# Performance work log

Hardware: AMD Instinct MI355X
Metric: run time of the kernel (lower is better)

The kernel has to match this reference:

```python
import jax, jax.numpy as jnp
import numpy as np

N = 1024          # num_rois == nongt_dim
FEAT = 1024       # feat_dim
EMB = 64          # emb_dim
G = 16            # group == fc_dim
DG = FEAT // G    # dim_group = 64
CLS = 80          # coco classes
EPS_POS = 1e-3
EPS_AFF = 1e-6


def setup_inputs() -> dict:
    key = jax.random.key(0)
    ks = jax.random.split(key, 12)
    # valid boxes: xmin,ymin in [0,500), width/height in [1,101)
    xymin = jax.random.uniform(ks[0], (N, 2), dtype=jnp.float32) * 500.0
    wh = 1.0 + jax.random.uniform(ks[1], (N, 2), dtype=jnp.float32) * 100.0
    bbox = jnp.concatenate([xymin[:, :1], xymin[:, 1:], xymin[:, :1] + wh[:, :1], xymin[:, 1:] + wh[:, 1:]], axis=1)
    roi_feat = jax.random.normal(ks[2], (N, FEAT), dtype=jnp.float32)
    s = lambda d: 1.0 / np.sqrt(d)
    return {
        "bbox": bbox,
        "roi_feat": roi_feat,
        "W_pos": jax.random.normal(ks[3], (EMB, G), dtype=jnp.float32) * s(EMB),
        "b_pos": jnp.zeros((G,), jnp.float32),
        "Wq": jax.random.normal(ks[4], (FEAT, FEAT), dtype=jnp.float32) * s(FEAT),
        "bq": jnp.zeros((FEAT,), jnp.float32),
        "Wk": jax.random.normal(ks[5], (FEAT, FEAT), dtype=jnp.float32) * s(FEAT),
        "bk": jnp.zeros((FEAT,), jnp.float32),
        # grouped 1x1 conv: groups=16, in/group=FEAT=1024, out/group=DG=64 -> [G, DG, FEAT]
        "W_conv": jax.random.normal(ks[6], (G, DG, FEAT), dtype=jnp.float32) * s(FEAT),
        "b_conv": jnp.zeros((FEAT,), jnp.float32),
        "W_ro": jax.random.normal(ks[7], (FEAT, CLS), dtype=jnp.float32) * s(FEAT),
        "b_ro": jnp.zeros((CLS,), jnp.float32),
    }


def _position_matrix(bbox):
    xmin, ymin, xmax, ymax = bbox[:, 0], bbox[:, 1], bbox[:, 2], bbox[:, 3]
    w = xmax - xmin + 1.0
    h = ymax - ymin + 1.0
    cx = 0.5 * (xmin + xmax)
    cy = 0.5 * (ymin + ymax)

    def log_clamped(d):
        d = jnp.where(jnp.abs(d) < EPS_POS, EPS_POS, d)
        return jnp.log(jnp.abs(d))

    dx = log_clamped((cx[:, None] - cx[None, :]) / w[:, None])
    dy = log_clamped((cy[:, None] - cy[None, :]) / h[:, None])
    dw = log_clamped(w[:, None] / w[None, :])
    dh = log_clamped(h[:, None] / h[None, :])
    return jnp.stack([dx, dy, dw, dh], axis=2)  # [N, N, 4]


def _position_embedding(pos_mat, feat_dim=EMB, wave_length=1000.0):
    feat_range = jnp.arange(feat_dim // 8, dtype=jnp.float32)          # 8 freqs
    dim_mat = jnp.power(jnp.float32(wave_length), (8.0 / feat_dim) * feat_range)
    div = pos_mat[..., None] / dim_mat                                  # [N, N, 4, 8]
    emb = jnp.concatenate([jnp.sin(div), jnp.cos(div)], axis=-1)        # [N, N, 4, 16]
    return emb.reshape(pos_mat.shape[0], pos_mat.shape[1], feat_dim)    # [N, N, 64]


def reference(bbox, roi_feat, W_pos, b_pos, Wq, bq, Wk, bk, W_conv, b_conv, W_ro, b_ro):
    n = roi_feat.shape[0]
    pos_emb = _position_embedding(_position_matrix(bbox))               # [N, N, 64]
    aff_w = jax.nn.relu(pos_emb @ W_pos + b_pos)                        # [N, N, G]
    aff_w = jnp.transpose(aff_w, (0, 2, 1))                             # [N, G, N]

    q = (roi_feat @ Wq + bq).reshape(n, G, DG)                          # [N, G, DG]
    k = (roi_feat @ Wk + bk).reshape(n, G, DG)
    aff = jnp.einsum('igd,jgd->igj', q, k) * (1.0 / np.sqrt(DG))        # [N, G, N]

    aff_w = jnp.where(aff_w < EPS_AFF, EPS_AFF, aff_w)
    sm = jax.nn.softmax(jnp.log(aff_w) + aff, axis=2)                   # [N, G, N]

    out_t = jnp.einsum('igj,jd->igd', sm, roi_feat)                     # [N, G, FEAT]
    lin = jnp.einsum('igd,gkd->igk', out_t, W_conv).reshape(n, FEAT) + b_conv
    res = roi_feat + lin                                                # [N, FEAT]
    logits = res.sum(axis=0, keepdims=True) @ W_ro + b_ro               # [1, CLS]
    return jax.nn.sigmoid(logits)
```

## Files before the change

kernel.cpp:

```cpp
#include <hip/hip_runtime.h>
#include <hip/hip_bf16.h>
#include <math.h>

#define NN   1024
#define GG   16
#define DGD  64
#define CLS  80
#define SPLIT 4
#define JT_PER 4

typedef __attribute__((ext_vector_type(8))) short short8;
typedef __attribute__((ext_vector_type(4))) float f32x4;
typedef _Float16 half8 __attribute__((ext_vector_type(8)));

__device__ inline void split2t(float x, ushort& h, ushort& l) {
  uint u = __float_as_uint(x);
  h = (ushort)(u >> 16);
  float r = x - __uint_as_float(u & 0xFFFF0000u);
  l = (ushort)(__float_as_uint(r) >> 16);
}

__device__ inline ushort f32tof16(float x) {
  _Float16 h = (_Float16)x;
  return *(ushort*)&h;
}
__device__ inline float f16tof32(ushort u) {
  _Float16 h; *(ushort*)&h = u;
  return (float)h;
}

__device__ inline int wslot(int r, int kc) {
  return ((r >> 4) << 6) + ((kc & 3) << 4) + ((r & 15) ^ ((kc & 3) << 2));
}
__device__ inline int rslot(int f, int lane) {
  return (f << 6) + ((lane >> 4) << 4) + ((lane & 15) ^ ((lane >> 4) << 2));
}

__global__ __launch_bounds__(256) void prep_k(
    const float* __restrict__ roi, ushort* __restrict__ roiH, ushort* __restrict__ roiL,
    const float* __restrict__ Wc,  ushort* __restrict__ WcH,  ushort* __restrict__ WcL,
    const float* __restrict__ Wq,  const float* __restrict__ Wk,
    ushort* __restrict__ WqTH, ushort* __restrict__ WqTL,
    ushort* __restrict__ WkTH, ushort* __restrict__ WkTL)
{
  __shared__ float Tl[64][68];
  const int bid = blockIdx.x;
  const int t = threadIdx.x;

  if (bid < 512) {
    const float* src = bid < 256 ? roi : Wc;
    ushort* H = bid < 256 ? roiH : WcH;
    ushort* L = bid < 256 ? roiL : WcL;
    const int base = ((bid & 255) * 256 + t) * 16;
    float v[16];
    *(float4*)&v[0]  = *(const float4*)&src[base];
    *(float4*)&v[4]  = *(const float4*)&src[base + 4];
    *(float4*)&v[8]  = *(const float4*)&src[base + 8];
    *(float4*)&v[12] = *(const float4*)&src[base + 12];
    ushort hs[16], ls[16];
#pragma unroll
    for (int u = 0; u < 16; ++u) split2t(v[u], hs[u], ls[u]);
    *(uint4*)&H[base]     = *(uint4*)&hs[0];
    *(uint4*)&H[base + 8] = *(uint4*)&hs[8];
    *(uint4*)&L[base]     = *(uint4*)&ls[0];
    *(uint4*)&L[base + 8] = *(uint4*)&ls[8];
  } else {
    const int s = bid - 512;
    const float* W = (s >> 8) ? Wk : Wq;
    ushort* H = (s >> 8) ? WkTH : WqTH;
    ushort* L = (s >> 8) ? WkTL : WqTL;
    const int rb = s & 255;
    const int j0 = (rb & 15) * 64, k0 = (rb >> 4) * 64;
    const int r = t >> 2, c = (t & 3) * 16;
#pragma unroll
    for (int u = 0; u < 4; ++u)
      *(float4*)&Tl[r][c + u * 4] = *(const float4*)&W[(k0 + r) * NN + j0 + c + u * 4];
    __syncthreads();
    ushort hs[16], ls[16];
#pragma unroll
    for (int u = 0; u < 16; ++u) split2t(Tl[c + u][r], hs[u], ls[u]);
    const int ob = (j0 + r) * NN + k0 + c;
    *(uint4*)&H[ob]     = *(uint4*)&hs[0];
    *(uint4*)&H[ob + 8] = *(uint4*)&hs[8];
    *(uint4*)&L[ob]     = *(uint4*)&ls[0];
    *(uint4*)&L[ob + 8] = *(uint4*)&ls[8];
  }
}

__global__ __launch_bounds__(256) void fused_m(
    const float* __restrict__ bbox, const float* __restrict__ Wp,
    const float* __restrict__ bp,
    const ushort* __restrict__ roiH, const ushort* __restrict__ roiL,
    const ushort* __restrict__ WqTH, const ushort* __restrict__ WqTL,
    const ushort* __restrict__ WkTH, const ushort* __restrict__ WkTL,
    const ushort* __restrict__ WcH,  const ushort* __restrict__ WcL,
    const float* __restrict__ bq, const float* __restrict__ bk,
    ushort* __restrict__ qHp, ushort* __restrict__ qLp,
    ushort* __restrict__ kHp, ushort* __restrict__ kLp,
    ushort* __restrict__ rwHp, ushort* __restrict__ rwLp,
    ushort* __restrict__ paffh)
{
  __shared__ short8 sAH[256], sAL[256], sBH[256], sBL[256];
  const int bid = blockIdx.x;
  const int t = threadIdx.x, lane = t & 63, w = t >> 6;

  if (bid % 14 < 6) {
    const int gi = (bid / 14) * 6 + (bid % 14);
    const int crow = (lane >> 4) * 4, ccol = lane & 15;
    const int kc = t & 3, r = t >> 2;
    const int sl0 = wslot(r, kc);
    const int wr = w >> 1, wc = w & 1;

    const ushort *AH_, *AL_, *BH_, *BL_;
    const float* bias;
    ushort *OH_, *OL_;
    int j0;
    if (gi < 512) {
      const int z = gi >> 8, rb = gi & 255;
      const int i0 = (rb >> 4) * 64;
      j0 = (rb & 15) * 64;
      AH_ = roiH + (size_t)i0 * NN;
      AL_ = roiL + (size_t)i0 * NN;
      BH_ = z ? WkTH : WqTH;
      BL_ = z ? WkTL : WqTL;
      bias = z ? bk : bq;
      OH_ = (z ? kHp : qHp) + (size_t)i0 * NN;
      OL_ = (z ? kLp : qLp) + (size_t)i0 * NN;
    } else {
      const int s = gi - 512;
      const int g = s >> 4;
      j0 = (s & 15) * 64;
      AH_ = WcH + (size_t)g * DGD * NN;
      AL_ = WcL + (size_t)g * DGD * NN;
      BH_ = roiH;
      BL_ = roiL;
      bias = nullptr;
      OH_ = rwHp + (size_t)g * DGD * NN;
      OL_ = rwLp + (size_t)g * DGD * NN;
    }

    uint4 vah, val, vbh, vbl;
#define LOADT(kt) { const int ka = (kt) * 32 + (kc << 3); \
    vah = *(const uint4*)&AH_[(size_t)r * NN + ka]; \
    val = *(const uint4*)&AL_[(size_t)r * NN + ka]; \
    vbh = *(const uint4*)&BH_[(size_t)(j0 + r) * NN + ka]; \
    vbl = *(const uint4*)&BL_[(size_t)(j0 + r) * NN + ka]; }

    LOADT(0);
    f32x4 acc[2][2] = {};
    for (int kt = 0; kt < 32; ++kt) {
      __syncthreads();
      *(uint4*)&sAH[sl0] = vah; *(uint4*)&sAL[sl0] = val;
      *(uint4*)&sBH[sl0] = vbh; *(uint4*)&sBL[sl0] = vbl;
      __syncthreads();
      if (kt + 1 < 32) LOADT(kt + 1);
      short8 ah[2], al[2], bh[2], bl[2];
#pragma unroll
      for (int f = 0; f < 2; ++f) {
        ah[f] = sAH[rslot(wr * 2 + f, lane)];
        al[f] = sAL[rslot(wr * 2 + f, lane)];
        bh[f] = sBH[rslot(wc * 2 + f, lane)];
        bl[f] = sBL[rslot(wc * 2 + f, lane)];
      }
#pragma unroll
      for (int fm = 0; fm < 2; ++fm)
#pragma unroll
        for (int fn = 0; fn < 2; ++fn) {
          acc[fm][fn] = __builtin_amdgcn_mfma_f32_16x16x32_bf16(ah[fm], bh[fn], acc[fm][fn], 0, 0, 0);
          acc[fm][fn] = __builtin_amdgcn_mfma_f32_16x16x32_bf16(ah[fm], bl[fn], acc[fm][fn], 0, 0, 0);
          acc[fm][fn] = __builtin_amdgcn_mfma_f32_16x16x32_bf16(al[fm], bh[fn], acc[fm][fn], 0, 0, 0);
        }
    }
#undef LOADT
#pragma unroll
    for (int fm = 0; fm < 2; ++fm) {
      const int row = wr * 32 + fm * 16 + crow;
#pragma unroll
      for (int fn = 0; fn < 2; ++fn) {
        const int col = j0 + wc * 32 + fn * 16 + ccol;
        const float bb = bias ? bias[col] : 0.0f;
#pragma unroll
        for (int e = 0; e < 4; ++e) {
          ushort hh, ll; split2t(acc[fm][fn][e] + bb, hh, ll);
          OH_[(size_t)(row + e) * NN + col] = hh;
          OL_[(size_t)(row + e) * NN + col] = ll;
        }
      }
    }
  } else {
    const int i = (bid / 14) * 8 + (bid % 14) - 6;
    half8* sWH = (half8*)sAH;
    half8* sWL = (half8*)sAL;
    float* bpS = (float*)sBH;

    if (t < 128) {
      const int h = t >> 6, kc2 = (t >> 4) & 3, g = t & 15;
      _Float16 hh[8], ll[8];
#pragma unroll
      for (int u = 0; u < 8; ++u) {
        float x = Wp[(h * 32 + kc2 * 8 + u) * 16 + g];
        _Float16 xh = (_Float16)x;
        hh[u] = xh;
        ll[u] = (_Float16)(x - (float)xh);
      }
      sWH[t] = *(half8*)&hh[0];
      sWL[t] = *(half8*)&ll[0];
    }
    if (t < 16) bpS[t] = bp[t];
    __syncthreads();

    const half8 wh0 = sWH[lane], wh1 = sWH[64 + lane];
    const half8 wl0 = sWL[lane], wl1 = sWL[64 + lane];
    const float bb = bpS[lane & 15];

    const float xi0 = bbox[i*4+0], yi0 = bbox[i*4+1], xi1 = bbox[i*4+2], yi1 = bbox[i*4+3];
    const float wi = xi1 - xi0 + 1.0f, hi = yi1 - yi0 + 1.0f;
    const float cxi = 0.5f*(xi0+xi1), cyi = 0.5f*(yi0+yi1);

    const int jr = lane & 15, p = lane >> 4;
    const int csel = p >> 1;
    const bool iscos = (p & 1);
    const float shift = iscos ? 1.5707963267948966f : 0.0f;

    const float invdim[8] = {1.0f, 0.42169650342858224f, 0.17782794100389228f,
        0.07498942093324558f, 0.03162277660168379f, 0.01333521432163324f,
        0.005623413251903491f, 0.0023713737056616554f};

#pragma unroll 1
    for (int f = 0; f < 16; ++f) {
      const int j0 = w * 256 + f * 16;
      float4 bj = *(const float4*)&bbox[(j0 + jr) * 4];
      const float wj = bj.z - bj.x + 1.0f, hj = bj.w - bj.y + 1.0f;
      const float cxj = 0.5f*(bj.x+bj.z), cyj = 0.5f*(bj.y+bj.w);

      const float num1 = csel ? (cyi - cyj) : (cxi - cxj);
      const float den1 = csel ? hi : wi;
      const float pos1 = __logf(fmaxf(fabsf(num1 / den1), 1e-3f));
      const float num2 = csel ? hi : wi;
      const float den2 = csel ? hj : wj;
      const float pos2 = __logf(fmaxf(fabsf(num2 / den2), 1e-3f));

      _Float16 a1[8], a2[8];
#pragma unroll
      for (int u = 0; u < 4; ++u) {
        a1[u] = (_Float16)__sinf(fmaf(pos1, invdim[u], shift));
        a2[u] = (_Float16)__sinf(fmaf(pos2, invdim[u], shift));
      }
#pragma unroll
      for (int u = 4; u < 8; ++u) {
        const float b1 = pos1 * invdim[u];
        const float b2 = pos2 * invdim[u];
        const float q1 = b1 * b1, q2 = b2 * b2;
        const float s1 = b1 * fmaf(q1, -0.16666667f, 1.0f);
        const float c1 = fmaf(q1, -0.5f, 1.0f);
        const float s2 = b2 * fmaf(q2, -0.16666667f, 1.0f);
        const float c2 = fmaf(q2, -0.5f, 1.0f);
        a1[u] = (_Float16)(iscos ? c1 : s1);
        a2[u] = (_Float16)(iscos ? c2 : s2);
      }
      const half8 A1 = *(half8*)&a1[0];
      const half8 A2 = *(half8*)&a2[0];

      f32x4 acc = {0.f, 0.f, 0.f, 0.f};
      acc = __builtin_amdgcn_mfma_f32_16x16x32_f16(A1, wh0, acc, 0, 0, 0);
      acc = __builtin_amdgcn_mfma_f32_16x16x32_f16(A2, wh1, acc, 0, 0, 0);
      acc = __builtin_amdgcn_mfma_f32_16x16x32_f16(A1, wl0, acc, 0, 0, 0);
      acc = __builtin_amdgcn_mfma_f32_16x16x32_f16(A2, wl1, acc, 0, 0, 0);

      ushort o4[4];
      o4[0] = f32tof16(__logf(fmaxf(acc[0] + bb, 1e-6f)));
      o4[1] = f32tof16(__logf(fmaxf(acc[1] + bb, 1e-6f)));
      o4[2] = f32tof16(__logf(fmaxf(acc[2] + bb, 1e-6f)));
      o4[3] = f32tof16(__logf(fmaxf(acc[3] + bb, 1e-6f)));
      *(short4*)&paffh[((i * GG + (lane & 15)) << 10) + j0 + p * 4] = *(short4*)&o4[0];
    }
  }
}

__global__ __launch_bounds__(256) void attn_m(
    const ushort* __restrict__ qhp, const ushort* __restrict__ qlp,
    const ushort* __restrict__ khp, const ushort* __restrict__ klp,
    const ushort* __restrict__ rwhp, const ushort* __restrict__ rwlp,
    const ushort* __restrict__ paffh,
    float* __restrict__ po, float* __restrict__ pstat)
{
  const int g  = blockIdx.y;
  const int i0 = blockIdx.x * 64;
  const int sp = blockIdx.z;
  const int t  = threadIdx.x;
  const int lane = t & 63, w = t >> 6;

  __shared__ short8 sKH[512], sKL[512], sRH[512], sRL[512];
  __shared__ float PT[4][16][68];

  const int r  = t >> 2;
  const int kc = t & 3;
  const int sl = wslot(r, kc);

  {
    const ushort* s0 = qhp + (size_t)(i0 + r) * NN + g * DGD + kc * 8;
    const ushort* s1 = qlp + (size_t)(i0 + r) * NN + g * DGD + kc * 8;
    *(uint4*)&sKH[sl]       = *(const uint4*)&s0[0];
    *(uint4*)&sKH[sl + 256] = *(const uint4*)&s0[32];
    *(uint4*)&sKL[sl]       = *(const uint4*)&s1[0];
    *(uint4*)&sKL[sl + 256] = *(const uint4*)&s1[32];
  }
  __syncthreads();
  const int qsl = rslot(w, lane);
  const short8 qf_h0 = sKH[qsl], qf_h1 = sKH[256 + qsl];
  const short8 qf_l0 = sKL[qsl], qf_l1 = sKL[256 + qsl];

  const int qr = (lane >> 4) * 4;
  const int qc = lane & 15;

  float m[4], l[4];
  f32x4 o[4] = {};
#pragma unroll
  for (int e = 0; e < 4; ++e) { m[e] = -1e30f; l[e] = 0.f; }

#pragma unroll 1
  for (int jt = sp * JT_PER; jt < sp * JT_PER + JT_PER; ++jt) {
    const int j0 = jt * 64;
    const ushort* ks0 = khp + (size_t)(j0 + r) * NN + g * DGD + kc * 8;
    const ushort* ks1 = klp + (size_t)(j0 + r) * NN + g * DGD + kc * 8;
    uint4 kv00 = *(const uint4*)&ks0[0], kv01 = *(const uint4*)&ks0[32];
    uint4 kv10 = *(const uint4*)&ks1[0], kv11 = *(const uint4*)&ks1[32];
    const ushort* rs0 = rwhp + ((size_t)g * DGD + r) * NN + j0 + kc * 8;
    const ushort* rs1 = rwlp + ((size_t)g * DGD + r) * NN + j0 + kc * 8;
    uint4 rv00 = *(const uint4*)&rs0[0], rv01 = *(const uint4*)&rs0[32];
    uint4 rv10 = *(const uint4*)&rs1[0], rv11 = *(const uint4*)&rs1[32];
    float pf[4][4];
#pragma unroll
    for (int jf = 0; jf < 4; ++jf)
#pragma unroll
      for (int e = 0; e < 4; ++e)
        pf[jf][e] = f16tof32(paffh[(((i0 + w * 16 + qr + e) * GG + g) << 10) + j0 + jf * 16 + qc]);

    __syncthreads();
    *(uint4*)&sKH[sl] = kv00; *(uint4*)&sKH[sl + 256] = kv01;
    *(uint4*)&sKL[sl] = kv10; *(uint4*)&sKL[sl + 256] = kv11;
    *(uint4*)&sRH[sl] = rv00; *(uint4*)&sRH[sl + 256] = rv01;
    *(uint4*)&sRL[sl] = rv10; *(uint4*)&sRL[sl + 256] = rv11;
    __syncthreads();

    f32x4 s4[4];
#pragma unroll
    for (int jf = 0; jf < 4; ++jf) {
      const int bs = rslot(jf, lane);
      short8 bh0 = sKH[bs], bh1 = sKH[256 + bs];
      short8 bl0 = sKL[bs], bl1 = sKL[256 + bs];
      f32x4 a = {0.f, 0.f, 0.f, 0.f};
      a = __builtin_amdgcn_mfma_f32_16x16x32_bf16(qf_h0, bh0, a, 0, 0, 0);
      a = __builtin_amdgcn_mfma_f32_16x16x32_bf16(qf_h1, bh1, a, 0, 0, 0);
      a = __builtin_amdgcn_mfma_f32_16x16x32_bf16(qf_h0, bl0, a, 0, 0, 0);
      a = __builtin_amdgcn_mfma_f32_16x16x32_bf16(qf_h1, bl1, a, 0, 0, 0);
      a = __builtin_amdgcn_mfma_f32_16x16x32_bf16(qf_l0, bh0, a, 0, 0, 0);
      a = __builtin_amdgcn_mfma_f32_16x16x32_bf16(qf_l1, bh1, a, 0, 0, 0);
      s4[jf] = a;
    }

#pragma unroll
    for (int e = 0; e < 4; ++e) {
      float v0 = fmaf(s4[0][e], 0.125f, pf[0][e]);
      float v1 = fmaf(s4[1][e], 0.125f, pf[1][e]);
      float v2 = fmaf(s4[2][e], 0.125f, pf[2][e]);
      float v3 = fmaf(s4[3][e], 0.125f, pf[3][e]);
      float tm = fmaxf(fmaxf(v0, v1), fmaxf(v2, v3));
#pragma unroll
      for (int off = 1; off < 16; off <<= 1) tm = fmaxf(tm, __shfl_xor(tm, off, 64));
      const float mn = fmaxf(m[e], tm);
      const float sc = __expf(m[e] - mn);
      v0 = __expf(v0 - mn); v1 = __expf(v1 - mn);
      v2 = __expf(v2 - mn); v3 = __expf(v3 - mn);
      float ts = (v0 + v1) + (v2 + v3);
#pragma unroll
      for (int off = 1; off < 16; off <<= 1) ts += __shfl_xor(ts, off, 64);
      l[e] = l[e] * sc + ts;
      m[e] = mn;
#pragma unroll
      for (int nf = 0; nf < 4; ++nf) o[nf][e] *= sc;
      PT[w][qr + e][ 0 + qc] = v0;
      PT[w][qr + e][16 + qc] = v1;
      PT[w][qr + e][32 + qc] = v2;
      PT[w][qr + e][48 + qc] = v3;
    }

    short8 ph[2], pl[2];
#pragma unroll
    for (int h = 0; h < 2; ++h) {
      const float* psrc = &PT[w][lane & 15][h * 32 + (lane >> 4) * 8];
      float4 x = *(const float4*)&psrc[0];
      float4 y = *(const float4*)&psrc[4];
      float vv[8] = {x.x, x.y, x.z, x.w, y.x, y.y, y.z, y.w};
      ushort hh[8], ll[8];
#pragma unroll
      for (int u = 0; u < 8; ++u) split2t(vv[u], hh[u], ll[u]);
      ph[h] = *(short8*)&hh[0];
      pl[h] = *(short8*)&ll[0];
    }

#pragma unroll
    for (int nf = 0; nf < 4; ++nf) {
      const int bs = rslot(nf, lane);
      short8 rh0 = sRH[bs], rh1 = sRH[256 + bs];
      short8 rl0 = sRL[bs], rl1 = sRL[256 + bs];
      f32x4 a = o[nf];
      a = __builtin_amdgcn_mfma_f32_16x16x32_bf16(ph[0], rh0, a, 0, 0, 0);
      a = __builtin_amdgcn_mfma_f32_16x16x32_bf16(ph[1], rh1, a, 0, 0, 0);
      a = __builtin_amdgcn_mfma_f32_16x16x32_bf16(ph[0], rl0, a, 0, 0, 0);
      a = __builtin_amdgcn_mfma_f32_16x16x32_bf16(ph[1], rl1, a, 0, 0, 0);
      a = __builtin_amdgcn_mfma_f32_16x16x32_bf16(pl[0], rh0, a, 0, 0, 0);
      a = __builtin_amdgcn_mfma_f32_16x16x32_bf16(pl[1], rh1, a, 0, 0, 0);
      o[nf] = a;
    }
  }

  const size_t idx = ((size_t)blockIdx.x * GG + g) * SPLIT + sp;
  float* pot = po + idx * 4096;
#pragma unroll
  for (int nf = 0; nf < 4; ++nf)
#pragma unroll
    for (int e = 0; e < 4; ++e)
      pot[(w * 16 + qr + e) * 64 + nf * 16 + qc] = o[nf][e];
  if (qc == 0) {
#pragma unroll
    for (int e = 0; e < 4; ++e) {
      const int row = w * 16 + qr + e;
      pstat[(idx * 64 + row) * 2]     = m[e];
      pstat[(idx * 64 + row) * 2 + 1] = l[e];
    }
  }
}

__global__ __launch_bounds__(256) void combine_k(
    const float* __restrict__ po, const float* __restrict__ pstat,
    const float* __restrict__ roi, const float* __restrict__ bconv,
    float* __restrict__ res)
{
  const int it = blockIdx.x, g = blockIdx.y;
  const int t = threadIdx.x;
  const int row = t >> 2, c0 = (t & 3) * 16;
  const size_t base = ((size_t)it * GG + g) * SPLIT;

  float ms[SPLIT], ls[SPLIT];
#pragma unroll
  for (int s = 0; s < SPLIT; ++s) {
    float2 st = *(const float2*)&pstat[((base + s) * 64 + row) * 2];
    ms[s] = st.x; ls[s] = st.y;
  }
  float M = ms[0];
#pragma unroll
  for (int s = 1; s < SPLIT; ++s) M = fmaxf(M, ms[s]);
  float wgt[SPLIT], L = 0.f;
#pragma unroll
  for (int s = 0; s < SPLIT; ++s) { wgt[s] = __expf(ms[s] - M); L = fmaf(ls[s], wgt[s], L); }
  const float rL = 1.0f / L;

  const int grow = it * 64 + row;
  const int f0   = g * DGD + c0;
#pragma unroll
  for (int c = 0; c < 4; ++c) {
    float4 acc = {0.f, 0.f, 0.f, 0.f};
#pragma unroll
    for (int s = 0; s < SPLIT; ++s) {
      float4 v = *(const float4*)&po[(base + s) * 4096 + row * 64 + c0 + c * 4];
      acc.x = fmaf(v.x, wgt[s], acc.x);
      acc.y = fmaf(v.y, wgt[s], acc.y);
      acc.z = fmaf(v.z, wgt[s], acc.z);
      acc.w = fmaf(v.w, wgt[s], acc.w);
    }
    float4 r4 = *(const float4*)&roi[grow * NN + f0 + c * 4];
    float4 b4 = *(const float4*)&bconv[f0 + c * 4];
    float4 ov;
    ov.x = r4.x + b4.x + acc.x * rL;
    ov.y = r4.y + b4.y + acc.y * rL;
    ov.z = r4.z + b4.z + acc.z * rL;
    ov.w = r4.w + b4.w + acc.w * rL;
    *(float4*)&res[grow * NN + f0 + c * 4] = ov;
  }
}

__global__ __launch_bounds__(256) void colsum_partial_k(
    const float* __restrict__ res, float* __restrict__ part)
{
  const int d  = blockIdx.x * 256 + threadIdx.x;
  const int r0 = blockIdx.y * 128;
  float s0 = 0.f, s1 = 0.f, s2 = 0.f, s3 = 0.f;
  for (int i = 0; i < 128; i += 4) {
    s0 += res[(r0 + i    ) * NN + d];
    s1 += res[(r0 + i + 1) * NN + d];
    s2 += res[(r0 + i + 2) * NN + d];
    s3 += res[(r0 + i + 3) * NN + d];
  }
  part[blockIdx.y * NN + d] = (s0 + s1) + (s2 + s3);
}

__global__ __launch_bounds__(640) void final_k(
    const float* __restrict__ part, const float* __restrict__ W_ro,
    const float* __restrict__ b_ro, float* __restrict__ out)
{
  __shared__ float cs[1024];
  __shared__ float red[8][CLS];
  const int t = threadIdx.x;

  for (int u = t; u < 1024; u += 640) {
    float s = 0.f;
#pragma unroll
    for (int p = 0; p < 8; ++p) s += part[p * NN + u];
    cs[u] = s;
  }
  __syncthreads();

  {
    const int c = t % CLS, s = t / CLS;
    float acc = 0.f;
    const int d0 = s * 128;
#pragma unroll 8
    for (int d = d0; d < d0 + 128; ++d)
      acc = fmaf(cs[d], W_ro[d * CLS + c], acc);
    red[s][c] = acc;
  }
  __syncthreads();

  if (t < CLS) {
    float lg = b_ro[t];
#pragma unroll
    for (int s = 0; s < 8; ++s) lg += red[s][t];
    out[t] = 1.0f / (1.0f + __expf(-lg));
  }
}

extern "C" void kernel_launch(void* const* d_in, const int* in_sizes, int n_in,
                              void* d_out, int out_size, void* d_ws, size_t ws_size,
                              hipStream_t stream) {
  const float* bbox  = (const float*)d_in[0];
  const float* roi   = (const float*)d_in[1];
  const float* W_pos = (const float*)d_in[2];
  const float* b_pos = (const float*)d_in[3];
  const float* Wq    = (const float*)d_in[4];
  const float* bq    = (const float*)d_in[5];
  const float* Wk    = (const float*)d_in[6];
  const float* bk    = (const float*)d_in[7];
  const float* Wc    = (const float*)d_in[8];
  const float* bcv   = (const float*)d_in[9];
  const float* W_ro  = (const float*)d_in[10];
  const float* b_ro  = (const float*)d_in[11];

  float* ws = (float*)d_ws;
  ushort* paffh = (ushort*)ws;
  float* po = ws + (8 << 20);
  ushort* roiH = (ushort*)(ws + (16 << 20));
  ushort* roiL = (ushort*)(ws + (16 << 20) + (1 << 19));
  ushort* WqTH = (ushort*)(ws + (17 << 20));
  ushort* WqTL = (ushort*)(ws + (17 << 20) + (1 << 19));
  ushort* WkTH = (ushort*)(ws + (18 << 20));
  ushort* WkTL = (ushort*)(ws + (18 << 20) + (1 << 19));
  ushort* WcH  = (ushort*)(ws + (19 << 20));
  ushort* WcL  = (ushort*)(ws + (19 << 20) + (1 << 19));
  ushort* qHp  = (ushort*)(ws + (20 << 20));
  ushort* qLp  = (ushort*)(ws + (20 << 20) + (1 << 19));
  ushort* kHp  = (ushort*)(ws + (21 << 20));
  ushort* kLp  = (ushort*)(ws + (21 << 20) + (1 << 19));
  ushort* rwHp = (ushort*)(ws + (22 << 20));
  ushort* rwLp = (ushort*)(ws + (22 << 20) + (1 << 19));
  float* pstat = ws + (23 << 20);
  float* part  = ws + (23 << 20) + (1 << 18);
  float* res   = ws + (23 << 20) + (1 << 19);

  prep_k<<<1024, 256, 0, stream>>>(roi, roiH, roiL, Wc, WcH, WcL,
                                   Wq, Wk, WqTH, WqTL, WkTH, WkTL);

  fused_m<<<1792, 256, 0, stream>>>(bbox, W_pos, b_pos,
                                    roiH, roiL, WqTH, WqTL, WkTH, WkTL,
                                    WcH, WcL, bq, bk,
                                    qHp, qLp, kHp, kLp, rwHp, rwLp, paffh);

  attn_m<<<dim3(16, 16, SPLIT), 256, 0, stream>>>(qHp, qLp, kHp, kLp, rwHp, rwLp,
                                                  paffh, po, pstat);
  combine_k<<<dim3(16, 16), 256, 0, stream>>>(po, pstat, roi, bcv, res);
  colsum_partial_k<<<dim3(4, 8), 256, 0, stream>>>(res, part);
  final_k<<<1, 640, 0, stream>>>(part, W_ro, b_ro, (float*)d_out);
}
```

Measured before the change: 111.6 us.

## Double-buffer GEMM register prefetch and fuse column-sum into combine kernel

The GEMM loop in fused_m now keeps two sets of prefetch registers and unrolls by two, issuing each global load two K-steps ahead so more latency is hidden behind the MFMA work. Separately, combine_k now reduces its 64x64 output tile through shared memory into per-row-tile partial column sums, which removes the colsum_partial_k launch and its re-read of res. final_k then sums 16 partials instead of 8. The cost is higher register pressure in fused_m and extra shared memory plus a serial 64-step reduction in combine_k.

```diff
diff --git a/kernel.cpp b/kernel.cpp
--- a/kernel.cpp
+++ b/kernel.cpp
@@ -139,39 +139,54 @@
       OL_ = rwLp + (size_t)g * DGD * NN;
     }
 
-    uint4 vah, val, vbh, vbl;
-#define LOADT(kt) { const int ka = (kt) * 32 + (kc << 3); \
-    vah = *(const uint4*)&AH_[(size_t)r * NN + ka]; \
-    val = *(const uint4*)&AL_[(size_t)r * NN + ka]; \
-    vbh = *(const uint4*)&BH_[(size_t)(j0 + r) * NN + ka]; \
-    vbl = *(const uint4*)&BL_[(size_t)(j0 + r) * NN + ka]; }
-
-    LOADT(0);
+    uint4 vahA, valA, vbhA, vblA, vahB, valB, vbhB, vblB;
+#define LOADTA(kt) { const int ka = (kt) * 32 + (kc << 3); \
+    vahA = *(const uint4*)&AH_[(size_t)r * NN + ka]; \
+    valA = *(const uint4*)&AL_[(size_t)r * NN + ka]; \
+    vbhA = *(const uint4*)&BH_[(size_t)(j0 + r) * NN + ka]; \
+    vblA = *(const uint4*)&BL_[(size_t)(j0 + r) * NN + ka]; }
+#define LOADTB(kt) { const int ka = (kt) * 32 + (kc << 3); \
+    vahB = *(const uint4*)&AH_[(size_t)r * NN + ka]; \
+    valB = *(const uint4*)&AL_[(size_t)r * NN + ka]; \
+    vbhB = *(const uint4*)&BH_[(size_t)(j0 + r) * NN + ka]; \
+    vblB = *(const uint4*)&BL_[(size_t)(j0 + r) * NN + ka]; }
+#define COMPUTE() { \
+    short8 ah[2], al[2], bh[2], bl[2]; \
+    _Pragma("unroll") \
+    for (int f = 0; f < 2; ++f) { \
+      ah[f] = sAH[rslot(wr * 2 + f, lane)]; \
+      al[f] = sAL[rslot(wr * 2 + f, lane)]; \
+      bh[f] = sBH[rslot(wc * 2 + f, lane)]; \
+      bl[f] = sBL[rslot(wc * 2 + f, lane)]; \
+    } \
+    _Pragma("unroll") \
+    for (int fm = 0; fm < 2; ++fm) \
+      _Pragma("unroll") \
+      for (int fn = 0; fn < 2; ++fn) { \
+        acc[fm][fn] = __builtin_amdgcn_mfma_f32_16x16x32_bf16(ah[fm], bh[fn], acc[fm][fn], 0, 0, 0); \
+        acc[fm][fn] = __builtin_amdgcn_mfma_f32_16x16x32_bf16(ah[fm], bl[fn], acc[fm][fn], 0, 0, 0); \
+        acc[fm][fn] = __builtin_amdgcn_mfma_f32_16x16x32_bf16(al[fm], bh[fn], acc[fm][fn], 0, 0, 0); \
+      } }
+
+    LOADTA(0); LOADTB(1);
     f32x4 acc[2][2] = {};
-    for (int kt = 0; kt < 32; ++kt) {
+    for (int kt = 0; kt < 32; kt += 2) {
       __syncthreads();
-      *(uint4*)&sAH[sl0] = vah; *(uint4*)&sAL[sl0] = val;
-      *(uint4*)&sBH[sl0] = vbh; *(uint4*)&sBL[sl0] = vbl;
+      *(uint4*)&sAH[sl0] = vahA; *(uint4*)&sAL[sl0] = valA;
+      *(uint4*)&sBH[sl0] = vbhA; *(uint4*)&sBL[sl0] = vblA;
       __syncthreads();
-      if (kt + 1 < 32) LOADT(kt + 1);
-      short8 ah[2], al[2], bh[2], bl[2];
-#pragma unroll
-      for (int f = 0; f < 2; ++f) {
-        ah[f] = sAH[rslot(wr * 2 + f, lane)];
-        al[f] = sAL[rslot(wr * 2 + f, lane)];
-        bh[f] = sBH[rslot(wc * 2 + f, lane)];
-        bl[f] = sBL[rslot(wc * 2 + f, lane)];
-      }
-#pragma unroll
-      for (int fm = 0; fm < 2; ++fm)
-#pragma unroll
-        for (int fn = 0; fn < 2; ++fn) {
-          acc[fm][fn] = __builtin_amdgcn_mfma_f32_16x16x32_bf16(ah[fm], bh[fn], acc[fm][fn], 0, 0, 0);
-          acc[fm][fn] = __builtin_amdgcn_mfma_f32_16x16x32_bf16(ah[fm], bl[fn], acc[fm][fn], 0, 0, 0);
-          acc[fm][fn] = __builtin_amdgcn_mfma_f32_16x16x32_bf16(al[fm], bh[fn], acc[fm][fn], 0, 0, 0);
-        }
-    }
-#undef LOADT
+      if (kt + 2 < 32) LOADTA(kt + 2);
+      COMPUTE();
+      __syncthreads();
+      *(uint4*)&sAH[sl0] = vahB; *(uint4*)&sAL[sl0] = valB;
+      *(uint4*)&sBH[sl0] = vbhB; *(uint4*)&sBL[sl0] = vblB;
+      __syncthreads();
+      if (kt + 3 < 32) LOADTB(kt + 3);
+      COMPUTE();
+    }
+#undef LOADTA
+#undef LOADTB
+#undef COMPUTE
 #pragma unroll
     for (int fm = 0; fm < 2; ++fm) {
       const int row = wr * 32 + fm * 16 + crow;
@@ -435,8 +450,9 @@
 __global__ __launch_bounds__(256) void combine_k(
     const float* __restrict__ po, const float* __restrict__ pstat,
     const float* __restrict__ roi, const float* __restrict__ bconv,
-    float* __restrict__ res)
+    float* __restrict__ res, float* __restrict__ part2)
 {
+  __shared__ float T[64][68];
   const int it = blockIdx.x, g = blockIdx.y;
   const int t = threadIdx.x;
   const int row = t >> 2, c0 = (t & 3) * 16;
@@ -477,26 +493,19 @@
     ov.z = r4.z + b4.z + acc.z * rL;
     ov.w = r4.w + b4.w + acc.w * rL;
     *(float4*)&res[grow * NN + f0 + c * 4] = ov;
-  }
-}
-
-__global__ __launch_bounds__(256) void colsum_partial_k(
-    const float* __restrict__ res, float* __restrict__ part)
-{
-  const int d  = blockIdx.x * 256 + threadIdx.x;
-  const int r0 = blockIdx.y * 128;
-  float s0 = 0.f, s1 = 0.f, s2 = 0.f, s3 = 0.f;
-  for (int i = 0; i < 128; i += 4) {
-    s0 += res[(r0 + i    ) * NN + d];
-    s1 += res[(r0 + i + 1) * NN + d];
-    s2 += res[(r0 + i + 2) * NN + d];
-    s3 += res[(r0 + i + 3) * NN + d];
-  }
-  part[blockIdx.y * NN + d] = (s0 + s1) + (s2 + s3);
+    *(float4*)&T[row][c0 + c * 4] = ov;
+  }
+  __syncthreads();
+  if (t < 64) {
+    float s = 0.f;
+#pragma unroll 8
+    for (int rr = 0; rr < 64; ++rr) s += T[rr][t];
+    part2[(size_t)it * NN + g * DGD + t] = s;
+  }
 }
 
 __global__ __launch_bounds__(640) void final_k(
-    const float* __restrict__ part, const float* __restrict__ W_ro,
+    const float* __restrict__ part2, const float* __restrict__ W_ro,
     const float* __restrict__ b_ro, float* __restrict__ out)
 {
   __shared__ float cs[1024];
@@ -506,7 +515,7 @@
   for (int u = t; u < 1024; u += 640) {
     float s = 0.f;
 #pragma unroll
-    for (int p = 0; p < 8; ++p) s += part[p * NN + u];
+    for (int p = 0; p < 16; ++p) s += part2[(size_t)p * NN + u];
     cs[u] = s;
   }
   __syncthreads();
@@ -564,7 +573,7 @@
   ushort* rwHp = (ushort*)(ws + (22 << 20));
   ushort* rwLp = (ushort*)(ws + (22 << 20) + (1 << 19));
   float* pstat = ws + (23 << 20);
-  float* part  = ws + (23 << 20) + (1 << 18);
+  float* part2 = ws + (23 << 20) + (1 << 18);
   float* res   = ws + (23 << 20) + (1 << 19);
 
   prep_k<<<1024, 256, 0, stream>>>(roi, roiH, roiL, Wc, WcH, WcL,
@@ -577,7 +586,6 @@
 
   attn_m<<<dim3(16, 16, SPLIT), 256, 0, stream>>>(qHp, qLp, kHp, kLp, rwHp, rwLp,
                                                   paffh, po, pstat);
-  combine_k<<<dim3(16, 16), 256, 0, stream>>>(po, pstat, roi, bcv, res);
-  colsum_partial_k<<<dim3(4, 8), 256, 0, stream>>>(res, part);
-  final_k<<<1, 640, 0, stream>>>(part, W_ro, b_ro, (float*)d_out);
-}
+  combine_k<<<dim3(16, 16), 256, 0, stream>>>(po, pstat, roi, bcv, res, part2);
+  final_k<<<1, 640, 0, stream>>>(part2, W_ro, b_ro, (float*)d_out);
+}
```

Result: slower. 116.2 us (+4.1%).
